# Optimization experiments

Hardware: AMD Instinct MI355X
Metric: run time of the kernel (lower is better)

Reference implementation:

```python
import jax, jax.numpy as jnp
import numpy as np

N = 10000   # num_nodes
E = 320000  # num_edges
D = 256     # feature / hidden dim
H = 256


def adj_lap(edge_index, n):
    """Dense normalized adjacency (gcn_norm, no self loops) and sym Laplacian."""
    row, col = edge_index[0], edge_index[1]
    # dense 0/1 adjacency (duplicate edges overwrite with same value, as in the loop)
    A = jnp.zeros((n, n), dtype=jnp.float32).at[row, col].set(1.0)
    # gcn_norm: deg = scatter(w, col) -> column sums
    deg_c = A.sum(axis=0)
    dinv_c = jnp.where(deg_c > 0, jax.lax.rsqrt(jnp.maximum(deg_c, 1e-12)), 0.0)
    anorm = dinv_c[:, None] * A * dinv_c[None, :]
    # get_laplacian 'sym': deg = scatter(w, row) -> row sums; L = I - D^-1/2 A D^-1/2
    deg_r = A.sum(axis=1)
    dinv_r = jnp.where(deg_r > 0, jax.lax.rsqrt(jnp.maximum(deg_r, 1e-12)), 0.0)
    lap = jnp.eye(n, dtype=jnp.float32) - dinv_r[:, None] * A * dinv_r[None, :]
    return lap, anorm


def gcn2(x, M, W1, b1, W2, b2):
    # pretrain_model: two-layer spectral GCN using propagation matrix M
    h = jax.nn.relu(M @ (x @ W1) + b1)
    return M @ (h @ W2) + b2


def setup_inputs() -> dict:
    key = jax.random.key(0)
    k1, k2, k3, k4 = jax.random.split(key, 4)
    x = jax.random.normal(k1, (N, D), dtype=jnp.float32)
    edge_index = jax.random.randint(k2, (2, E), 0, N, dtype=jnp.int64)
    W1 = jax.random.normal(k3, (D, H), dtype=jnp.float32) * 0.05
    b1 = jnp.zeros((H,), dtype=jnp.float32)
    W2 = jax.random.normal(k4, (H, H), dtype=jnp.float32) * 0.05
    b2 = jnp.zeros((H,), dtype=jnp.float32)
    return {"x": x, "edge_index": edge_index, "W1": W1, "b1": b1, "W2": W2, "b2": b2}


def reference(x, edge_index, W1, b1, W2, b2):
    # identity augmentor: x1 = x2 = x, edge_index1 = edge_index2 = edge_index,
    # so adj_lap is identical for both branches (computed once).
    lsym, anorm = adj_lap(edge_index, x.shape[0])
    z1 = gcn2(x, lsym, W1, b1, W2, b2)   # 'high' pass
    z2 = gcn2(x, anorm, W1, b1, W2, b2)  # 'low' pass
    z = z2
    return (z, z1, z2)
```

## Files before the change

### kernel.cpp

```cpp
#include <hip/hip_runtime.h>

#define NN 10000
#define EE 320000
#define HH 256
#define BKT 192

typedef __attribute__((ext_vector_type(8))) short bf16x8;
typedef __attribute__((ext_vector_type(4))) float f32x4;

__device__ float bf2f(unsigned int v) {
    return __uint_as_float(v << 16);
}
__device__ unsigned short f2bf(float f) {
    unsigned int i = __float_as_uint(f);
    return (unsigned short)((i + 0x7fffu + ((i >> 16) & 1u)) >> 16);
}
__device__ unsigned int fp8e(float f) {
    float a = fabsf(f);
    a = fminf(a, 448.0f);
    unsigned int bits = __float_as_uint(a * __uint_as_float(0x03800000u));
    bits = bits + 0x7ffffu + ((bits >> 20) & 1u);
    unsigned int r = bits >> 20;
    if (r > 0x7eu) r = 0x7eu;
    return r | ((__float_as_uint(f) >> 24) & 0x80u);
}
__device__ float fp8d(unsigned int b) {
    float mag = __uint_as_float((b & 0x7fu) << 20) * __uint_as_float(0x7B800000u);
    return __uint_as_float(((b & 0x80u) << 24) | __float_as_uint(mag));
}
__device__ unsigned int pk2(unsigned short a, unsigned short b) {
    return (unsigned int)a | ((unsigned int)b << 16);
}
__device__ int eload(const void* ei, int is64, int idx) {
    if (is64) return (int)(((const long long*)ei)[idx]);
    return ((const int*)ei)[idx];
}
__device__ __forceinline__ float dinv_of(int d) {
    return d > 0 ? rsqrtf((float)d) : 0.0f;
}

__global__ void k_A(const void* x, const void* ei, const void* W1, const void* W2,
                    int* flags, int* rawcnt, unsigned short* W1sw,
                    unsigned short* W2sw) {
    int b = blockIdx.x, t = threadIdx.x;
    if (b >= 65) {
        int idx = (b - 65) * 256 + t;
        ((uint4*)rawcnt)[idx] = make_uint4(0, 0, 0, 0);
        return;
    }
    if (b == 0) {
        __shared__ int s0, s1;
        if (t == 0) { s0 = 0; s1 = 0; }
        __syncthreads();
        if (t < 64) {
            const unsigned int* eu = (const unsigned int*)ei;
            const unsigned int* xu = (const unsigned int*)x;
            for (int k = t; k < 256; k += 64)
                if (eu[2 * k + 1] != 0) atomicOr(&s0, 1);
            unsigned int lo = xu[t] & 0xffffu;
            unsigned int ex = (lo >> 7) & 0xffu;
            if (lo == 0u || (ex >= 90u && ex <= 150u)) atomicAdd(&s1, 1);
        }
        __syncthreads();
        if (t == 0) {
            flags[0] = s0 ? 0 : 1;
            flags[1] = (s1 >= 56) ? 0 : 1;
        }
        return;
    }
    __shared__ int plaus;
    if (t == 0) plaus = 0;
    __syncthreads();
    if (t < 64) {
        unsigned int lo = ((const unsigned int*)x)[t] & 0xffffu;
        unsigned int ex = (lo >> 7) & 0xffu;
        if (lo == 0u || (ex >= 90u && ex <= 150u)) atomicAdd(&plaus, 1);
    }
    __syncthreads();
    int f32io = (plaus >= 56) ? 0 : 1;
    int vb = b - 1;
    const void* W = (vb < 32) ? W1 : W2;
    unsigned short* O = (vb < 32) ? W1sw : W2sw;
    int g = ((vb < 32) ? vb : vb - 32) * 256 + t;
    int gl = g & 63;
    int n = (g >> 6) & 15;
    int ks = g >> 10;
    int coln = n * 16 + (gl & 15);
    int krow = ks * 32 + ((gl >> 4) & 3) * 8;
    unsigned short v[8];
    if (f32io) {
        const float* Wf = (const float*)W;
        #pragma unroll
        for (int j = 0; j < 8; j++) v[j] = f2bf(Wf[(size_t)(krow + j) * HH + coln]);
    } else {
        const unsigned short* Wh = (const unsigned short*)W;
        #pragma unroll
        for (int j = 0; j < 8; j++) v[j] = Wh[(size_t)(krow + j) * HH + coln];
    }
    uint4 p;
    p.x = pk2(v[0], v[1]); p.y = pk2(v[2], v[3]);
    p.z = pk2(v[4], v[5]); p.w = pk2(v[6], v[7]);
    *(uint4*)(O + (size_t)g * 8) = p;
}

__global__ void k_B(const void* x, const void* ei, const unsigned short* W1sw,
                    const int* flags, int* rawcnt, unsigned short* bucket,
                    unsigned char* Yf8, void* Oout) {
    int b = blockIdx.x;
    int tid = threadIdx.x;
    if (b >= 625) {
        int e = (b - 625) * 256 + tid;
        if (e >= EE) return;
        int is64 = flags[0];
        int r = eload(ei, is64, e);
        int c = eload(ei, is64, EE + e);
        if (r < 0 || r >= NN || c < 0 || c >= NN) return;
        int slot = atomicAdd(&rawcnt[r], 1);
        if (slot < BKT) bucket[(size_t)r * BKT + slot] = (unsigned short)c;
        return;
    }
    __shared__ unsigned short As[16][264];
    int r0 = b * 16;
    int af32 = flags[1];
    {
        int row = tid >> 4, seg = tid & 15;
        if (af32) {
            const float* ap = (const float*)x + (size_t)(r0 + row) * HH + seg * 16;
            unsigned short v[16];
            #pragma unroll
            for (int j = 0; j < 16; j += 4) {
                float4 q = *(const float4*)(ap + j);
                v[j] = f2bf(q.x); v[j + 1] = f2bf(q.y);
                v[j + 2] = f2bf(q.z); v[j + 3] = f2bf(q.w);
            }
            uint4 p0, p1;
            p0.x = pk2(v[0], v[1]);   p0.y = pk2(v[2], v[3]);
            p0.z = pk2(v[4], v[5]);   p0.w = pk2(v[6], v[7]);
            p1.x = pk2(v[8], v[9]);   p1.y = pk2(v[10], v[11]);
            p1.z = pk2(v[12], v[13]); p1.w = pk2(v[14], v[15]);
            *(uint4*)&As[row][seg * 16] = p0;
            *(uint4*)&As[row][seg * 16 + 8] = p1;
        } else {
            const unsigned short* ap = (const unsigned short*)x + (size_t)(r0 + row) * HH + seg * 16;
            *(uint4*)&As[row][seg * 16] = *(const uint4*)ap;
            *(uint4*)&As[row][seg * 16 + 8] = *(const uint4*)(ap + 8);
        }
    }
    __syncthreads();
    int wv = tid >> 6;
    int lane = tid & 63;
    int quad = lane >> 4;
    int l16 = lane & 15;
    f32x4 acc[4] = {{0,0,0,0},{0,0,0,0},{0,0,0,0},{0,0,0,0}};
    for (int ks = 0; ks < 8; ks++) {
        bf16x8 af = *(const bf16x8*)&As[l16][ks * 32 + quad * 8];
        #pragma unroll
        for (int t = 0; t < 4; t++) {
            int n = wv * 4 + t;
            bf16x8 bf = *(const bf16x8*)(W1sw + ((size_t)(ks * 16 + n) * 64 + lane) * 8);
            acc[t] = __builtin_amdgcn_mfma_f32_16x16x32_bf16(af, bf, acc[t], 0, 0, 0);
        }
    }
    size_t chunkW = (size_t)NN * HH;
    #pragma unroll
    for (int t = 0; t < 4; t++) {
        int cn = (wv * 4 + t) * 16 + l16;
        #pragma unroll
        for (int r = 0; r < 4; r++) {
            int row = r0 + quad * 4 + r;
            float vv = acc[t][r];
            size_t idx = (size_t)row * HH + cn;
            Yf8[idx] = (unsigned char)fp8e(vv);
            if (af32) ((float*)Oout)[2 * chunkW + idx] = vv;
            else      ((unsigned short*)Oout)[2 * chunkW + idx] = f2bf(vv);
        }
    }
}

__global__ void k_DD(const int* rawcnt, int* cnt2, unsigned short* bucket) {
    __shared__ unsigned int bm[4][316];
    __shared__ int cnt[4];
    int wave = threadIdx.x >> 6;
    int lane = threadIdx.x & 63;
    int i = blockIdx.x * 4 + wave;
    int d = rawcnt[i];
    if (d > BKT) d = BKT;
    for (int t = lane; t < 313; t += 64) bm[wave][t] = 0u;
    if (lane == 0) cnt[wave] = 0;
    unsigned short* bp = bucket + (size_t)i * BKT;
    int cvals[3];
    int nt = 0;
    for (int t = lane; t < d; t += 64) cvals[nt++] = (int)bp[t];
    for (int k = 0; k < nt; k++) {
        int c = cvals[k];
        unsigned int m = 1u << (c & 31);
        unsigned int old = atomicOr(&bm[wave][c >> 5], m);
        if (!(old & m)) {
            int p = atomicAdd(&cnt[wave], 1);
            bp[p] = (unsigned short)c;
            atomicAdd(&cnt2[2 * c + 1], 1);
        }
    }
    if (lane == 0) atomicExch(&cnt2[2 * i], cnt[wave]);
}

__global__ __launch_bounds__(512) void k_CD(
        const unsigned char* Yf8, const unsigned short* bucket,
        const int* cnt2, const unsigned short* W2sw, const void* b1,
        const int* flags, unsigned char* G12f8, void* Oout) {
    __shared__ unsigned short H1s[16][264];
    __shared__ unsigned short H2s[16][264];
    int tid = threadIdx.x;
    int wave = tid >> 6;
    int lane = tid & 63;
    int fb = lane * 4;
    int bbase = blockIdx.x * 16;
    int f32io = flags[1];
    size_t chunkW = (size_t)NN * HH;
    float bv[4];
    if (f32io) {
        const float* bp = (const float*)b1 + fb;
        #pragma unroll
        for (int k = 0; k < 4; k++) bv[k] = bp[k];
    } else {
        uint2 br = *(const uint2*)((const unsigned short*)b1 + fb);
        bv[0] = bf2f(br.x & 0xffffu); bv[1] = bf2f(br.x >> 16);
        bv[2] = bf2f(br.y & 0xffffu); bv[3] = bf2f(br.y >> 16);
    }
    for (int rr = 0; rr < 2; rr++) {
        int lr = wave * 2 + rr;
        int i = bbase + lr;
        float a1[4] = {0, 0, 0, 0};
        float a2[4] = {0, 0, 0, 0};
        int2 ddi = *(const int2*)(cnt2 + 2 * i);
        int n = ddi.x;
        const unsigned short* cp = bucket + (size_t)i * BKT;
        int t = 0;
        for (; t + 4 <= n; t += 4) {
            ushort4 c4 = *(const ushort4*)(cp + t);
            int cx[4] = {(int)c4.x, (int)c4.y, (int)c4.z, (int)c4.w};
            float wx[4], wy[4];
            #pragma unroll
            for (int j = 0; j < 4; j++) {
                int2 dd = *(const int2*)(cnt2 + 2 * cx[j]);
                wx[j] = dinv_of(dd.x);
                wy[j] = dinv_of(dd.y);
            }
            unsigned int gv[4];
            #pragma unroll
            for (int j = 0; j < 4; j++)
                gv[j] = *(const unsigned int*)(Yf8 + (size_t)cx[j] * 256 + fb);
            #pragma unroll
            for (int j = 0; j < 4; j++) {
                #pragma unroll
                for (int k = 0; k < 4; k++) {
                    float y = fp8d((gv[j] >> (8 * k)) & 0xffu);
                    a1[k] += wx[j] * y;
                    a2[k] += wy[j] * y;
                }
            }
        }
        for (; t < n; t++) {
            int c = (int)cp[t];
            int2 dd = *(const int2*)(cnt2 + 2 * c);
            float wx = dinv_of(dd.x);
            float wy = dinv_of(dd.y);
            unsigned int g = *(const unsigned int*)(Yf8 + (size_t)c * 256 + fb);
            #pragma unroll
            for (int k = 0; k < 4; k++) {
                float y = fp8d((g >> (8 * k)) & 0xffu);
                a1[k] += wx * y;
                a2[k] += wy * y;
            }
        }
        float wiix = dinv_of(ddi.x);
        float wiiy = dinv_of(ddi.y);
        float yv[4];
        if (f32io) {
            const float* sp = (const float*)Oout + 2 * chunkW + (size_t)i * HH + fb;
            #pragma unroll
            for (int k = 0; k < 4; k++) yv[k] = sp[k];
        } else {
            uint2 yi = *(const uint2*)((const unsigned short*)Oout + 2 * chunkW + (size_t)i * HH + fb);
            yv[0] = bf2f(yi.x & 0xffffu); yv[1] = bf2f(yi.x >> 16);
            yv[2] = bf2f(yi.y & 0xffffu); yv[3] = bf2f(yi.y >> 16);
        }
        float h1[4], h2[4];
        #pragma unroll
        for (int k = 0; k < 4; k++) {
            h1[k] = fmaxf(0.f, yv[k] - wiix * a1[k] + bv[k]);
            h2[k] = fmaxf(0.f, wiiy * a2[k] + bv[k]);
        }
        uint2 p1, p2;
        p1.x = pk2(f2bf(h1[0]), f2bf(h1[1])); p1.y = pk2(f2bf(h1[2]), f2bf(h1[3]));
        p2.x = pk2(f2bf(h2[0]), f2bf(h2[1])); p2.y = pk2(f2bf(h2[2]), f2bf(h2[3]));
        *(uint2*)&H1s[lr][fb] = p1;
        *(uint2*)&H2s[lr][fb] = p2;
    }
    __syncthreads();
    int quad = lane >> 4;
    int l16 = lane & 15;
    f32x4 acc1[2] = {{0,0,0,0},{0,0,0,0}};
    f32x4 acc2[2] = {{0,0,0,0},{0,0,0,0}};
    for (int ks = 0; ks < 8; ks++) {
        bf16x8 af1 = *(const bf16x8*)&H1s[l16][ks * 32 + quad * 8];
        bf16x8 af2 = *(const bf16x8*)&H2s[l16][ks * 32 + quad * 8];
        #pragma unroll
        for (int t = 0; t < 2; t++) {
            int n = wave * 2 + t;
            bf16x8 bf = *(const bf16x8*)(W2sw + ((size_t)(ks * 16 + n) * 64 + lane) * 8);
            acc1[t] = __builtin_amdgcn_mfma_f32_16x16x32_bf16(af1, bf, acc1[t], 0, 0, 0);
            acc2[t] = __builtin_amdgcn_mfma_f32_16x16x32_bf16(af2, bf, acc2[t], 0, 0, 0);
        }
    }
    #pragma unroll
    for (int t = 0; t < 2; t++) {
        int cn = (wave * 2 + t) * 16 + l16;
        #pragma unroll
        for (int r = 0; r < 4; r++) {
            int row = bbase + quad * 4 + r;
            float v1 = acc1[t][r];
            float v2 = acc2[t][r];
            G12f8[(size_t)row * 512 + cn] = (unsigned char)fp8e(v1);
            G12f8[(size_t)row * 512 + 256 + cn] = (unsigned char)fp8e(v2);
            size_t idx = (size_t)row * HH + cn;
            if (f32io) ((float*)Oout)[chunkW + idx] = v1;
            else       ((unsigned short*)Oout)[chunkW + idx] = f2bf(v1);
        }
    }
}

__global__ void k_E(const unsigned char* G12f8, const unsigned short* bucket,
                    const int* cnt2, const void* bias, const int* flags,
                    void* Oout) {
    int wave = threadIdx.x >> 6;
    int lane = threadIdx.x & 63;
    int half = lane >> 5;
    int sub = lane & 31;
    int fb = sub * 8;
    int goff = half * 256 + fb;
    int i = blockIdx.x * 4 + wave;
    float acc[8] = {0, 0, 0, 0, 0, 0, 0, 0};
    int2 ddi = *(const int2*)(cnt2 + 2 * i);
    int n = ddi.x;
    const unsigned short* cp = bucket + (size_t)i * BKT;
    int t = 0;
    for (; t + 4 <= n; t += 4) {
        ushort4 c4 = *(const ushort4*)(cp + t);
        int cx[4] = {(int)c4.x, (int)c4.y, (int)c4.z, (int)c4.w};
        float ws[4];
        #pragma unroll
        for (int j = 0; j < 4; j++) {
            int2 dd = *(const int2*)(cnt2 + 2 * cx[j]);
            ws[j] = dinv_of(half ? dd.y : dd.x);
        }
        uint2 gv[4];
        #pragma unroll
        for (int j = 0; j < 4; j++)
            gv[j] = *(const uint2*)(G12f8 + (size_t)cx[j] * 512 + goff);
        #pragma unroll
        for (int j = 0; j < 4; j++) {
            #pragma unroll
            for (int k = 0; k < 4; k++) {
                float y = fp8d((gv[j].x >> (8 * k)) & 0xffu);
                acc[k] += ws[j] * y;
            }
            #pragma unroll
            for (int k = 0; k < 4; k++) {
                float y = fp8d((gv[j].y >> (8 * k)) & 0xffu);
                acc[4 + k] += ws[j] * y;
            }
        }
    }
    for (; t < n; t++) {
        int c = (int)cp[t];
        int2 dd = *(const int2*)(cnt2 + 2 * c);
        float wsel = dinv_of(half ? dd.y : dd.x);
        uint2 g = *(const uint2*)(G12f8 + (size_t)c * 512 + goff);
        #pragma unroll
        for (int k = 0; k < 4; k++) acc[k] += wsel * fp8d((g.x >> (8 * k)) & 0xffu);
        #pragma unroll
        for (int k = 0; k < 4; k++) acc[4 + k] += wsel * fp8d((g.y >> (8 * k)) & 0xffu);
    }
    int f32io = flags[1];
    float bv[8];
    if (f32io) {
        const float* bp = (const float*)bias + fb;
        #pragma unroll
        for (int k = 0; k < 8; k++) bv[k] = bp[k];
    } else {
        uint4 br = *(const uint4*)((const unsigned short*)bias + fb);
        bv[0] = bf2f(br.x & 0xffffu); bv[1] = bf2f(br.x >> 16);
        bv[2] = bf2f(br.y & 0xffffu); bv[3] = bf2f(br.y >> 16);
        bv[4] = bf2f(br.z & 0xffffu); bv[5] = bf2f(br.z >> 16);
        bv[6] = bf2f(br.w & 0xffffu); bv[7] = bf2f(br.w >> 16);
    }
    size_t base = (size_t)i * HH + fb;
    size_t chunkW = (size_t)NN * HH;
    float z[8];
    if (half == 0) {
        float wiix = dinv_of(ddi.x);
        float gvv[8];
        if (f32io) {
            const float* sp = (const float*)Oout + chunkW + base;
            #pragma unroll
            for (int k = 0; k < 8; k++) gvv[k] = sp[k];
        } else {
            uint4 gi = *(const uint4*)((const unsigned short*)Oout + chunkW + base);
            gvv[0] = bf2f(gi.x & 0xffffu); gvv[1] = bf2f(gi.x >> 16);
            gvv[2] = bf2f(gi.y & 0xffffu); gvv[3] = bf2f(gi.y >> 16);
            gvv[4] = bf2f(gi.z & 0xffffu); gvv[5] = bf2f(gi.z >> 16);
            gvv[6] = bf2f(gi.w & 0xffffu); gvv[7] = bf2f(gi.w >> 16);
        }
        #pragma unroll
        for (int k = 0; k < 8; k++) z[k] = gvv[k] - wiix * acc[k] + bv[k];
        if (f32io) {
            float* o = (float*)Oout + chunkW + base;
            *(float4*)o = make_float4(z[0], z[1], z[2], z[3]);
            *(float4*)(o + 4) = make_float4(z[4], z[5], z[6], z[7]);
        } else {
            uint4 p;
            p.x = pk2(f2bf(z[0]), f2bf(z[1])); p.y = pk2(f2bf(z[2]), f2bf(z[3]));
            p.z = pk2(f2bf(z[4]), f2bf(z[5])); p.w = pk2(f2bf(z[6]), f2bf(z[7]));
            *(uint4*)((unsigned short*)Oout + chunkW + base) = p;
        }
    } else {
        float wiiy = dinv_of(ddi.y);
        #pragma unroll
        for (int k = 0; k < 8; k++) z[k] = wiiy * acc[k] + bv[k];
        if (f32io) {
            float* o0 = (float*)Oout + base;
            float* o2 = (float*)Oout + 2 * chunkW + base;
            float4 pa = make_float4(z[0], z[1], z[2], z[3]);
            float4 pb = make_float4(z[4], z[5], z[6], z[7]);
            *(float4*)o0 = pa; *(float4*)(o0 + 4) = pb;
            *(float4*)o2 = pa; *(float4*)(o2 + 4) = pb;
        } else {
            uint4 p;
            p.x = pk2(f2bf(z[0]), f2bf(z[1])); p.y = pk2(f2bf(z[2]), f2bf(z[3]));
            p.z = pk2(f2bf(z[4]), f2bf(z[5])); p.w = pk2(f2bf(z[6]), f2bf(z[7]));
            *(uint4*)((unsigned short*)Oout + base) = p;
            *(uint4*)((unsigned short*)Oout + 2 * chunkW + base) = p;
        }
    }
}

extern "C" void kernel_launch(void* const* d_in, const int* in_sizes, int n_in,
                              void* d_out, int out_size, void* d_ws, size_t ws_size,
                              hipStream_t stream) {
    const void* x = 0; const void* ei = 0;
    const void* W1 = 0; const void* b1 = 0; const void* W2 = 0; const void* b2 = 0;
    for (int i = 0; i < n_in; i++) {
        int s = in_sizes[i];
        if (s == NN * HH) x = d_in[i];
        else if (s == 2 * EE) ei = d_in[i];
        else if (s == HH * HH) { if (!W1) W1 = d_in[i]; else W2 = d_in[i]; }
        else if (s == HH) { if (!b1) b1 = d_in[i]; else b2 = d_in[i]; }
    }

    char* ws = (char*)d_ws;
    size_t off = 0;
    int* flags = (int*)(ws + off); off += 256;
    int* rawcnt = (int*)(ws + off); off += 40960;
    int* cnt2 = (int*)(ws + off); off += 81920;
    unsigned short* bucket = (unsigned short*)(ws + off); off += (size_t)NN * BKT * 2;
    unsigned short* W1sw = (unsigned short*)(ws + off); off += (size_t)HH * HH * 2;
    unsigned short* W2sw = (unsigned short*)(ws + off); off += (size_t)HH * HH * 2;
    unsigned char* Yf8 = (unsigned char*)(ws + off); off += (size_t)NN * 256;
    unsigned char* G12f8 = (unsigned char*)(ws + off); off += (size_t)NN * 512;

    k_A<<<95, 256, 0, stream>>>(x, ei, W1, W2, flags, rawcnt, W1sw, W2sw);
    k_B<<<1875, 256, 0, stream>>>(x, ei, W1sw, flags, rawcnt, bucket, Yf8, d_out);
    k_DD<<<NN / 4, 256, 0, stream>>>(rawcnt, cnt2, bucket);
    k_CD<<<625, 512, 0, stream>>>(Yf8, bucket, cnt2, W2sw, b1, flags, G12f8, d_out);
    k_E<<<NN / 4, 256, 0, stream>>>(G12f8, bucket, cnt2, b2, flags, d_out);
}
```

Measured before the change: 204.3 us.

## Halve rows per block in k_CD and decode fp8 with hardware conversions

k_CD now processes 8 nodes per block, one per wave, instead of 16 nodes with two per wave. The high-pass and low-pass hidden rows are stacked into a single 16-row bf16 tile, so each wave issues one MFMA chain instead of two, and the launch grid doubles to NN/8 blocks. Separately, fp8 decoding in k_CD and k_E goes through the packed cvt_pk_f32_fp8 builtin when it is available, replacing the manual bit-manipulation decode. The intent is to shorten the serial gather work per wave, get more parallelism for hiding latency, and cut ALU cost in the gather loops. The trade-off is that W2 fragments are reloaded by twice as many blocks, and the hardware decode must match the custom e4m3 encoding.

```diff
diff --git a/kernel.cpp b/kernel.cpp
--- a/kernel.cpp
+++ b/kernel.cpp
@@ -7,6 +7,7 @@
 
 typedef __attribute__((ext_vector_type(8))) short bf16x8;
 typedef __attribute__((ext_vector_type(4))) float f32x4;
+typedef __attribute__((ext_vector_type(2))) float f32x2;
 
 __device__ float bf2f(unsigned int v) {
     return __uint_as_float(v << 16);
@@ -27,6 +28,16 @@
 __device__ float fp8d(unsigned int b) {
     float mag = __uint_as_float((b & 0x7fu) << 20) * __uint_as_float(0x7B800000u);
     return __uint_as_float(((b & 0x80u) << 24) | __float_as_uint(mag));
+}
+__device__ __forceinline__ void fp8dec4(unsigned int g, float* o) {
+#if __has_builtin(__builtin_amdgcn_cvt_pk_f32_fp8)
+    f32x2 lo = __builtin_amdgcn_cvt_pk_f32_fp8((int)g, false);
+    f32x2 hi = __builtin_amdgcn_cvt_pk_f32_fp8((int)g, true);
+    o[0] = lo.x; o[1] = lo.y; o[2] = hi.x; o[3] = hi.y;
+#else
+    #pragma unroll
+    for (int j = 0; j < 4; j++) o[j] = fp8d((g >> (8 * j)) & 0xffu);
+#endif
 }
 __device__ unsigned int pk2(unsigned short a, unsigned short b) {
     return (unsigned int)a | ((unsigned int)b << 16);
@@ -204,17 +215,16 @@
     if (lane == 0) atomicExch(&cnt2[2 * i], cnt[wave]);
 }
 
-__global__ __launch_bounds__(512) void k_CD(
+__global__ __launch_bounds__(512, 8) void k_CD(
         const unsigned char* Yf8, const unsigned short* bucket,
         const int* cnt2, const unsigned short* W2sw, const void* b1,
         const int* flags, unsigned char* G12f8, void* Oout) {
-    __shared__ unsigned short H1s[16][264];
-    __shared__ unsigned short H2s[16][264];
+    __shared__ unsigned short Hs[16][264];
     int tid = threadIdx.x;
     int wave = tid >> 6;
     int lane = tid & 63;
     int fb = lane * 4;
-    int bbase = blockIdx.x * 16;
+    int bbase = blockIdx.x * 8;
     int f32io = flags[1];
     size_t chunkW = (size_t)NN * HH;
     float bv[4];
@@ -227,9 +237,8 @@
         bv[0] = bf2f(br.x & 0xffffu); bv[1] = bf2f(br.x >> 16);
         bv[2] = bf2f(br.y & 0xffffu); bv[3] = bf2f(br.y >> 16);
     }
-    for (int rr = 0; rr < 2; rr++) {
-        int lr = wave * 2 + rr;
-        int i = bbase + lr;
+    {
+        int i = bbase + wave;
         float a1[4] = {0, 0, 0, 0};
         float a2[4] = {0, 0, 0, 0};
         int2 ddi = *(const int2*)(cnt2 + 2 * i);
@@ -252,11 +261,12 @@
                 gv[j] = *(const unsigned int*)(Yf8 + (size_t)cx[j] * 256 + fb);
             #pragma unroll
             for (int j = 0; j < 4; j++) {
+                float y[4];
+                fp8dec4(gv[j], y);
                 #pragma unroll
                 for (int k = 0; k < 4; k++) {
-                    float y = fp8d((gv[j] >> (8 * k)) & 0xffu);
-                    a1[k] += wx[j] * y;
-                    a2[k] += wy[j] * y;
+                    a1[k] += wx[j] * y[k];
+                    a2[k] += wy[j] * y[k];
                 }
             }
         }
@@ -266,11 +276,12 @@
             float wx = dinv_of(dd.x);
             float wy = dinv_of(dd.y);
             unsigned int g = *(const unsigned int*)(Yf8 + (size_t)c * 256 + fb);
+            float y[4];
+            fp8dec4(g, y);
             #pragma unroll
             for (int k = 0; k < 4; k++) {
-                float y = fp8d((g >> (8 * k)) & 0xffu);
-                a1[k] += wx * y;
-                a2[k] += wy * y;
+                a1[k] += wx * y[k];
+                a2[k] += wy * y[k];
             }
         }
         float wiix = dinv_of(ddi.x);
@@ -294,23 +305,20 @@
         uint2 p1, p2;
         p1.x = pk2(f2bf(h1[0]), f2bf(h1[1])); p1.y = pk2(f2bf(h1[2]), f2bf(h1[3]));
         p2.x = pk2(f2bf(h2[0]), f2bf(h2[1])); p2.y = pk2(f2bf(h2[2]), f2bf(h2[3]));
-        *(uint2*)&H1s[lr][fb] = p1;
-        *(uint2*)&H2s[lr][fb] = p2;
+        *(uint2*)&Hs[wave][fb] = p1;
+        *(uint2*)&Hs[8 + wave][fb] = p2;
     }
     __syncthreads();
     int quad = lane >> 4;
     int l16 = lane & 15;
-    f32x4 acc1[2] = {{0,0,0,0},{0,0,0,0}};
-    f32x4 acc2[2] = {{0,0,0,0},{0,0,0,0}};
+    f32x4 acc[2] = {{0,0,0,0},{0,0,0,0}};
     for (int ks = 0; ks < 8; ks++) {
-        bf16x8 af1 = *(const bf16x8*)&H1s[l16][ks * 32 + quad * 8];
-        bf16x8 af2 = *(const bf16x8*)&H2s[l16][ks * 32 + quad * 8];
+        bf16x8 af = *(const bf16x8*)&Hs[l16][ks * 32 + quad * 8];
         #pragma unroll
         for (int t = 0; t < 2; t++) {
             int n = wave * 2 + t;
             bf16x8 bf = *(const bf16x8*)(W2sw + ((size_t)(ks * 16 + n) * 64 + lane) * 8);
-            acc1[t] = __builtin_amdgcn_mfma_f32_16x16x32_bf16(af1, bf, acc1[t], 0, 0, 0);
-            acc2[t] = __builtin_amdgcn_mfma_f32_16x16x32_bf16(af2, bf, acc2[t], 0, 0, 0);
+            acc[t] = __builtin_amdgcn_mfma_f32_16x16x32_bf16(af, bf, acc[t], 0, 0, 0);
         }
     }
     #pragma unroll
@@ -318,14 +326,18 @@
         int cn = (wave * 2 + t) * 16 + l16;
         #pragma unroll
         for (int r = 0; r < 4; r++) {
-            int row = bbase + quad * 4 + r;
-            float v1 = acc1[t][r];
-            float v2 = acc2[t][r];
-            G12f8[(size_t)row * 512 + cn] = (unsigned char)fp8e(v1);
-            G12f8[(size_t)row * 512 + 256 + cn] = (unsigned char)fp8e(v2);
-            size_t idx = (size_t)row * HH + cn;
-            if (f32io) ((float*)Oout)[chunkW + idx] = v1;
-            else       ((unsigned short*)Oout)[chunkW + idx] = f2bf(v1);
+            int row16 = quad * 4 + r;
+            float vv = acc[t][r];
+            if (row16 < 8) {
+                int node = bbase + row16;
+                G12f8[(size_t)node * 512 + cn] = (unsigned char)fp8e(vv);
+                size_t idx = (size_t)node * HH + cn;
+                if (f32io) ((float*)Oout)[chunkW + idx] = vv;
+                else       ((unsigned short*)Oout)[chunkW + idx] = f2bf(vv);
+            } else {
+                int node = bbase + row16 - 8;
+                G12f8[(size_t)node * 512 + 256 + cn] = (unsigned char)fp8e(vv);
+            }
         }
     }
 }
@@ -360,15 +372,13 @@
             gv[j] = *(const uint2*)(G12f8 + (size_t)cx[j] * 512 + goff);
         #pragma unroll
         for (int j = 0; j < 4; j++) {
+            float y[4], y2[4];
+            fp8dec4(gv[j].x, y);
+            fp8dec4(gv[j].y, y2);
             #pragma unroll
             for (int k = 0; k < 4; k++) {
-                float y = fp8d((gv[j].x >> (8 * k)) & 0xffu);
-                acc[k] += ws[j] * y;
-            }
-            #pragma unroll
-            for (int k = 0; k < 4; k++) {
-                float y = fp8d((gv[j].y >> (8 * k)) & 0xffu);
-                acc[4 + k] += ws[j] * y;
+                acc[k]     += ws[j] * y[k];
+                acc[4 + k] += ws[j] * y2[k];
             }
         }
     }
@@ -377,10 +387,14 @@
         int2 dd = *(const int2*)(cnt2 + 2 * c);
         float wsel = dinv_of(half ? dd.y : dd.x);
         uint2 g = *(const uint2*)(G12f8 + (size_t)c * 512 + goff);
-        #pragma unroll
-        for (int k = 0; k < 4; k++) acc[k] += wsel * fp8d((g.x >> (8 * k)) & 0xffu);
-        #pragma unroll
-        for (int k = 0; k < 4; k++) acc[4 + k] += wsel * fp8d((g.y >> (8 * k)) & 0xffu);
+        float y[4], y2[4];
+        fp8dec4(g.x, y);
+        fp8dec4(g.y, y2);
+        #pragma unroll
+        for (int k = 0; k < 4; k++) {
+            acc[k]     += wsel * y[k];
+            acc[4 + k] += wsel * y2[k];
+        }
     }
     int f32io = flags[1];
     float bv[8];
@@ -472,6 +486,6 @@
     k_A<<<95, 256, 0, stream>>>(x, ei, W1, W2, flags, rawcnt, W1sw, W2sw);
     k_B<<<1875, 256, 0, stream>>>(x, ei, W1sw, flags, rawcnt, bucket, Yf8, d_out);
     k_DD<<<NN / 4, 256, 0, stream>>>(rawcnt, cnt2, bucket);
-    k_CD<<<625, 512, 0, stream>>>(Yf8, bucket, cnt2, W2sw, b1, flags, G12f8, d_out);
+    k_CD<<<NN / 8, 512, 0, stream>>>(Yf8, bucket, cnt2, W2sw, b1, flags, G12f8, d_out);
     k_E<<<NN / 4, 256, 0, stream>>>(G12f8, bucket, cnt2, b2, flags, d_out);
 }
```

Measured after the change: 184.0 us. -9.9%, faster.
